# Kernel optimization log

Hardware: AMD Instinct MI355X
Metric: run time of the kernel (lower is better)

## Reference

```python
import jax, jax.numpy as jnp
import numpy as np

B, S, D, H = 4, 2048, 1024, 16
HD = D // H  # 64


def setup_inputs() -> dict:
    key = jax.random.key(0)
    k1, k2, k3 = jax.random.split(key, 3)
    return {
        "hidden_states": jax.random.normal(k1, (B, S, D), dtype=jnp.float32),
        "c_attn_w": jax.random.normal(k2, (D, 3 * D), dtype=jnp.float32) * 0.02,
        "c_attn_b": jnp.zeros((3 * D,), dtype=jnp.float32),
        "c_proj_w": jax.random.normal(k3, (D, D), dtype=jnp.float32) * 0.02,
        "c_proj_b": jnp.zeros((D,), dtype=jnp.float32),
    }


def reference(hidden_states, c_attn_w, c_attn_b, c_proj_w, c_proj_b):
    b, s, d = hidden_states.shape
    qkv = hidden_states @ c_attn_w + c_attn_b  # [B,S,3D]
    q, k, v = jnp.split(qkv, 3, axis=-1)
    # split heads -> [B,H,S,hd]
    def heads(x):
        return x.reshape(b, s, H, HD).transpose(0, 2, 1, 3)
    q, k, v = heads(q), heads(k), heads(v)
    scale = 1.0 / jnp.float32(HD) ** 0.5  # scale_attn_weights=True, no layer-idx scaling
    # fp32 scores (module forces float via autocast(False))
    w = jnp.einsum("bhqd,bhkd->bhqk", q.astype(jnp.float32), k.astype(jnp.float32)) * scale
    causal = jnp.tril(jnp.ones((s, s), dtype=bool))  # [S,S]
    mask_value = jnp.finfo(w.dtype).min
    w = jnp.where(causal[None, None], w, mask_value)
    w = jax.nn.softmax(w, axis=-1).astype(v.dtype)
    a = jnp.einsum("bhqk,bhkd->bhqd", w, v)  # [B,H,S,hd]
    a = a.transpose(0, 2, 1, 3).reshape(b, s, d)  # merge heads
    return a @ c_proj_w + c_proj_b
```

## Files before the change

kernel.cpp:

```cpp
#include <hip/hip_runtime.h>
#include <stdint.h>

typedef __bf16 bf16x8 __attribute__((ext_vector_type(8)));
typedef short s16x8 __attribute__((ext_vector_type(8)));
typedef float f32x4 __attribute__((ext_vector_type(4)));

__device__ __forceinline__ short f2bf(float f) {
  union { float f; uint32_t u; } c; c.f = f;
  uint32_t r = (c.u + 0x7fffu + ((c.u >> 16) & 1u)) >> 16;
  return (short)(uint16_t)r;
}

__device__ __forceinline__ void async_copy16(short* lds, const short* g) {
  __builtin_amdgcn_global_load_lds((const __attribute__((address_space(1))) void*)g,
                                   (__attribute__((address_space(3))) void*)lds,
                                   16, 0, 0);
}

__global__ __launch_bounds__(256) void cast_bf16_kernel(const float* __restrict__ in,
                                                        short* __restrict__ out) {
  int i = blockIdx.x * 256 + threadIdx.x;
  float4 v = reinterpret_cast<const float4*>(in)[i];
  short4 o;
  o.x = f2bf(v.x); o.y = f2bf(v.y); o.z = f2bf(v.z); o.w = f2bf(v.w);
  reinterpret_cast<short4*>(out)[i] = o;
}

__global__ __launch_bounds__(256) void transpose_cast_kernel(const float* __restrict__ in,
                                                             short* __restrict__ out,
                                                             int R, int C) {
  __shared__ float tile[32][33];
  int c0 = blockIdx.x * 32, r0 = blockIdx.y * 32;
  int tc = threadIdx.x & 31, tr = threadIdx.x >> 5;
#pragma unroll
  for (int p = 0; p < 4; ++p)
    tile[tr + p * 8][tc] = in[(size_t)(r0 + tr + p * 8) * C + c0 + tc];
  __syncthreads();
#pragma unroll
  for (int p = 0; p < 4; ++p)
    out[(size_t)(c0 + tr + p * 8) * R + r0 + tc] = f2bf(tile[tc][tr + p * 8]);
}

template <bool OBF, bool QSCALE>
__global__ __launch_bounds__(256) void gemm128_kernel(const short* __restrict__ A,
                                                      const short* __restrict__ Bt,
                                                      const float* __restrict__ bias,
                                                      void* __restrict__ Cout,
                                                      int K, int ldc) {
  __shared__ short Asm[128 * 32];
  __shared__ short Bsm[128 * 32];
  const int tid = threadIdx.x;
  const int lane = tid & 63, wid = tid >> 6;
  const int m0 = blockIdx.y * 128, n0 = blockIdx.x * 128;
  const int wm = wid >> 1, wn = wid & 1;
  const int lr = lane & 15, lg = lane >> 4;

  f32x4 acc[4][4] = {};

  const int s1 = tid, s2 = 256 + tid;
  const short* a1 = A + (size_t)(m0 + (s1 >> 2)) * K + (s1 & 3) * 8;
  const short* a2 = A + (size_t)(m0 + (s2 >> 2)) * K + (s2 & 3) * 8;
  const short* b1 = Bt + (size_t)(n0 + (s1 >> 2)) * K + (s1 & 3) * 8;
  const short* b2 = Bt + (size_t)(n0 + (s2 >> 2)) * K + (s2 & 3) * 8;

  for (int k0 = 0; k0 < K; k0 += 32) {
    __syncthreads();
    async_copy16(&Asm[s1 * 8], a1 + k0);
    async_copy16(&Asm[s2 * 8], a2 + k0);
    async_copy16(&Bsm[s1 * 8], b1 + k0);
    async_copy16(&Bsm[s2 * 8], b2 + k0);
    __syncthreads();

    bf16x8 af[4], bf[4];
#pragma unroll
    for (int mi = 0; mi < 4; ++mi)
      af[mi] = *(const bf16x8*)&Asm[(wm * 64 + mi * 16 + lr) * 32 + lg * 8];
#pragma unroll
    for (int ni = 0; ni < 4; ++ni)
      bf[ni] = *(const bf16x8*)&Bsm[(wn * 64 + ni * 16 + lr) * 32 + lg * 8];
    __builtin_amdgcn_s_setprio(1);
#pragma unroll
    for (int mi = 0; mi < 4; ++mi)
#pragma unroll
      for (int ni = 0; ni < 4; ++ni)
        acc[mi][ni] = __builtin_amdgcn_mfma_f32_16x16x32_bf16(af[mi], bf[ni], acc[mi][ni], 0, 0, 0);
    __builtin_amdgcn_s_setprio(0);
  }

#pragma unroll
  for (int ni = 0; ni < 4; ++ni) {
    const int col = n0 + wn * 64 + ni * 16 + lr;
    const float bv = bias[col];
    const float scale = (QSCALE && col < 1024) ? 0.18033688f : 1.0f;
#pragma unroll
    for (int mi = 0; mi < 4; ++mi) {
      const int row = m0 + wm * 64 + mi * 16 + lg * 4;
#pragma unroll
      for (int j = 0; j < 4; ++j) {
        const float v = (acc[mi][ni][j] + bv) * scale;
        if constexpr (OBF)
          ((short*)Cout)[(size_t)(row + j) * ldc + col] = f2bf(v);
        else
          ((float*)Cout)[(size_t)(row + j) * ldc + col] = v;
      }
    }
  }
}

__global__ __launch_bounds__(256) void vtrans_kernel(const short* __restrict__ qkv,
                                                     short* __restrict__ vt) {
  __shared__ short tile[64][72];
  const int tid = threadIdx.x;
  const int s0 = blockIdx.x * 64;
  const int h = blockIdx.y, b = blockIdx.z;
  const short* src = qkv + (size_t)(b * 2048 + s0) * 3072 + 2048 + h * 64;
#pragma unroll
  for (int p = 0; p < 2; ++p) {
    const int r = (tid >> 3) + p * 32;
    const int c0 = (tid & 7) * 8;
    *(s16x8*)&tile[r][c0] = *(const s16x8*)(src + (size_t)r * 3072 + c0);
  }
  __syncthreads();
  short* dst = vt + (size_t)(b * 16 + h) * 64 * 2048;
#pragma unroll
  for (int p = 0; p < 2; ++p) {
    const int d = (tid >> 3) + p * 32;
    const int sl0 = (tid & 7) * 8;
    s16x8 v;
#pragma unroll
    for (int i = 0; i < 8; ++i) v[i] = tile[sl0 + i][d];
    *(s16x8*)(dst + (size_t)d * 2048 + s0 + sl0) = v;
  }
}

__global__ __launch_bounds__(256) void attn_kernel(const short* __restrict__ qkv,
                                                   const short* __restrict__ vt,
                                                   short* __restrict__ abuf) {
  __shared__ short P_lds[4][32][72];
  const int tid = threadIdx.x;
  const int lane = tid & 63, wid = tid >> 6;
  const int lr = lane & 15, lg = lane >> 4;
  const int h = blockIdx.y, b = blockIdx.z;
  const int ldq = 3072;
  const short* Qb = qkv + (size_t)b * 2048 * ldq + h * 64;
  const short* Kb = Qb + 1024;
  const short* Vtb = vt + (size_t)(b * 16 + h) * 64 * 2048;

  for (int pp = 0; pp < 2; ++pp) {
    const int qtile = pp ? (int)blockIdx.x : 15 - (int)blockIdx.x;
    const int qrowA = qtile * 128 + wid * 32;

    bf16x8 qf[2][2];
#pragma unroll
    for (int qb = 0; qb < 2; ++qb)
#pragma unroll
      for (int g = 0; g < 2; ++g)
        qf[qb][g] = *(const bf16x8*)(Qb + (size_t)(qrowA + qb * 16 + lr) * ldq + g * 32 + lg * 8);

    f32x4 o[2][4] = {};
    float mst[2][4], lst[2][4];
#pragma unroll
    for (int qb = 0; qb < 2; ++qb)
#pragma unroll
      for (int j = 0; j < 4; ++j) { mst[qb][j] = -__builtin_inff(); lst[qb][j] = 0.f; }

    const int ntiles = ((qrowA + 31) >> 6) + 1;

    bf16x8 kf[4][2];
#pragma unroll
    for (int ni = 0; ni < 4; ++ni)
#pragma unroll
      for (int g = 0; g < 2; ++g)
        kf[ni][g] = *(const bf16x8*)(Kb + (size_t)(ni * 16 + lr) * ldq + g * 32 + lg * 8);

    for (int t = 0; t < ntiles; ++t) {
      const int kvt = t << 6;

      f32x4 s[2][4];
      __builtin_amdgcn_s_setprio(1);
#pragma unroll
      for (int qb = 0; qb < 2; ++qb)
#pragma unroll
        for (int ni = 0; ni < 4; ++ni) {
          f32x4 z = {0.f, 0.f, 0.f, 0.f};
          s[qb][ni] = z;
#pragma unroll
          for (int g = 0; g < 2; ++g)
            s[qb][ni] = __builtin_amdgcn_mfma_f32_16x16x32_bf16(qf[qb][g], kf[ni][g], s[qb][ni], 0, 0, 0);
        }
      __builtin_amdgcn_s_setprio(0);

      bf16x8 kn[4][2];
      if (t + 1 < ntiles) {
        const int kvn = kvt + 64;
#pragma unroll
        for (int ni = 0; ni < 4; ++ni)
#pragma unroll
          for (int g = 0; g < 2; ++g)
            kn[ni][g] = *(const bf16x8*)(Kb + (size_t)(kvn + ni * 16 + lr) * ldq + g * 32 + lg * 8);
      }
      bf16x8 vb[4][2];
#pragma unroll
      for (int db = 0; db < 4; ++db)
#pragma unroll
        for (int g = 0; g < 2; ++g)
          vb[db][g] = *(const bf16x8*)(Vtb + (size_t)(db * 16 + lr) * 2048 + kvt + g * 32 + lg * 8);

      if (kvt + 63 > qrowA) {
#pragma unroll
        for (int qb = 0; qb < 2; ++qb)
#pragma unroll
          for (int ni = 0; ni < 4; ++ni)
#pragma unroll
            for (int j = 0; j < 4; ++j) {
              const int q = qrowA + qb * 16 + lg * 4 + j;
              const int kv = kvt + ni * 16 + lr;
              if (kv > q) s[qb][ni][j] = -__builtin_inff();
            }
      }

      float alpha[2][4];
#pragma unroll
      for (int qb = 0; qb < 2; ++qb)
#pragma unroll
        for (int j = 0; j < 4; ++j) {
          float v = fmaxf(fmaxf(s[qb][0][j], s[qb][1][j]), fmaxf(s[qb][2][j], s[qb][3][j]));
          v = fmaxf(v, __shfl_xor(v, 1, 64));
          v = fmaxf(v, __shfl_xor(v, 2, 64));
          v = fmaxf(v, __shfl_xor(v, 4, 64));
          v = fmaxf(v, __shfl_xor(v, 8, 64));
          const float mn = fmaxf(mst[qb][j], v);
          alpha[qb][j] = exp2f(mst[qb][j] - mn);
          mst[qb][j] = mn;
          lst[qb][j] *= alpha[qb][j];
        }

#pragma unroll
      for (int qb = 0; qb < 2; ++qb)
#pragma unroll
        for (int db = 0; db < 4; ++db)
#pragma unroll
          for (int j = 0; j < 4; ++j)
            o[qb][db][j] *= alpha[qb][j];

      float psum[2][4] = {};
#pragma unroll
      for (int qb = 0; qb < 2; ++qb)
#pragma unroll
        for (int ni = 0; ni < 4; ++ni)
#pragma unroll
          for (int j = 0; j < 4; ++j) {
            const float p = exp2f(s[qb][ni][j] - mst[qb][j]);
            psum[qb][j] += p;
            P_lds[wid][qb * 16 + lg * 4 + j][ni * 16 + lr] = f2bf(p);
          }
#pragma unroll
      for (int qb = 0; qb < 2; ++qb)
#pragma unroll
        for (int j = 0; j < 4; ++j) {
          float v = psum[qb][j];
          v += __shfl_xor(v, 1, 64);
          v += __shfl_xor(v, 2, 64);
          v += __shfl_xor(v, 4, 64);
          v += __shfl_xor(v, 8, 64);
          lst[qb][j] += v;
        }

      bf16x8 pa[2][2];
#pragma unroll
      for (int qb = 0; qb < 2; ++qb)
#pragma unroll
        for (int g = 0; g < 2; ++g)
          pa[qb][g] = *(const bf16x8*)&P_lds[wid][qb * 16 + lr][g * 32 + lg * 8];

      __builtin_amdgcn_s_setprio(1);
#pragma unroll
      for (int qb = 0; qb < 2; ++qb)
#pragma unroll
        for (int db = 0; db < 4; ++db)
#pragma unroll
          for (int g = 0; g < 2; ++g)
            o[qb][db] = __builtin_amdgcn_mfma_f32_16x16x32_bf16(pa[qb][g], vb[db][g], o[qb][db], 0, 0, 0);
      __builtin_amdgcn_s_setprio(0);

#pragma unroll
      for (int ni = 0; ni < 4; ++ni)
#pragma unroll
        for (int g = 0; g < 2; ++g)
          kf[ni][g] = kn[ni][g];
    }

#pragma unroll
    for (int qb = 0; qb < 2; ++qb) {
      float rl[4];
#pragma unroll
      for (int j = 0; j < 4; ++j) rl[j] = 1.0f / lst[qb][j];
#pragma unroll
      for (int db = 0; db < 4; ++db) {
        const int col = h * 64 + db * 16 + lr;
#pragma unroll
        for (int j = 0; j < 4; ++j) {
          const int row = b * 2048 + qrowA + qb * 16 + lg * 4 + j;
          abuf[(size_t)row * 1024 + col] = f2bf(o[qb][db][j] * rl[j]);
        }
      }
    }
  }
}

extern "C" void kernel_launch(void* const* d_in, const int* in_sizes, int n_in,
                              void* d_out, int out_size, void* d_ws, size_t ws_size,
                              hipStream_t stream) {
  (void)in_sizes; (void)n_in; (void)out_size; (void)ws_size;
  const float* hs = (const float*)d_in[0];
  const float* w1 = (const float*)d_in[1];
  const float* b1 = (const float*)d_in[2];
  const float* w2 = (const float*)d_in[3];
  const float* b2 = (const float*)d_in[4];

  char* w = (char*)d_ws;
  short* Xb  = (short*)(w);
  short* W1T = (short*)(w + 16777216);
  short* W2T = (short*)(w + 23068672);
  short* QKV = (short*)(w + 25165824);
  short* VT  = (short*)(w + 75497472);
  short* AB  = (short*)(w + 92274688);

  cast_bf16_kernel<<<8192, 256, 0, stream>>>(hs, Xb);
  transpose_cast_kernel<<<dim3(96, 32), 256, 0, stream>>>(w1, W1T, 1024, 3072);
  transpose_cast_kernel<<<dim3(32, 32), 256, 0, stream>>>(w2, W2T, 1024, 1024);
  gemm128_kernel<true, true><<<dim3(24, 64), 256, 0, stream>>>(Xb, W1T, b1, QKV, 1024, 3072);
  vtrans_kernel<<<dim3(32, 16, 4), 256, 0, stream>>>(QKV, VT);
  attn_kernel<<<dim3(8, 16, 4), 256, 0, stream>>>(QKV, VT, AB);
  gemm128_kernel<false, false><<<dim3(8, 64), 256, 0, stream>>>(AB, W2T, b2, d_out, 1024, 1024);
}
```

Baseline: 388.9 us.

## Halve attention query tile per wave, remap grid, add lazy softmax rescaling

The attention kernel now gives each wave 16 query rows instead of 32, with each block covering a pair of 64-row subtiles. This doubles the grid to 1024 blocks, and a swizzled 1D block index maps blocks to (batch, head, tile) so that neighbouring blocks spread across heads. The online softmax now skips rescaling the max and the accumulators unless some row's max grows by more than 8 (log2 units), which removes exp and multiply work on most tiles. The bf16 conversion uses the native cast instead of manual rounding. The trade-offs are that K and V are reloaded per 16 rows, which doubles the global traffic for K and V, and that the lazy rescale depends on the bounded growth of the scores.

```diff
diff --git a/kernel.cpp b/kernel.cpp
--- a/kernel.cpp
+++ b/kernel.cpp
@@ -6,9 +6,9 @@
 typedef float f32x4 __attribute__((ext_vector_type(4)));
 
 __device__ __forceinline__ short f2bf(float f) {
-  union { float f; uint32_t u; } c; c.f = f;
-  uint32_t r = (c.u + 0x7fffu + ((c.u >> 16) & 1u)) >> 16;
-  return (short)(uint16_t)r;
+  union { __bf16 h; short s; } u;
+  u.h = (__bf16)f;
+  return u.s;
 }
 
 __device__ __forceinline__ void async_copy16(short* lds, const short* g) {
@@ -136,58 +136,56 @@
 __global__ __launch_bounds__(256) void attn_kernel(const short* __restrict__ qkv,
                                                    const short* __restrict__ vt,
                                                    short* __restrict__ abuf) {
-  __shared__ short P_lds[4][32][72];
+  __shared__ short P_lds[4][16][72];
   const int tid = threadIdx.x;
   const int lane = tid & 63, wid = tid >> 6;
   const int lr = lane & 15, lg = lane >> 4;
-  const int h = blockIdx.y, b = blockIdx.z;
+
+  const int g = blockIdx.x;
+  const int w = ((g & 7) << 7) | (g >> 3);
+  const int px = w & 15, h = (w >> 4) & 15, b = w >> 8;
+
   const int ldq = 3072;
   const short* Qb = qkv + (size_t)b * 2048 * ldq + h * 64;
   const short* Kb = Qb + 1024;
   const short* Vtb = vt + (size_t)(b * 16 + h) * 64 * 2048;
 
   for (int pp = 0; pp < 2; ++pp) {
-    const int qtile = pp ? (int)blockIdx.x : 15 - (int)blockIdx.x;
-    const int qrowA = qtile * 128 + wid * 32;
-
-    bf16x8 qf[2][2];
-#pragma unroll
-    for (int qb = 0; qb < 2; ++qb)
-#pragma unroll
-      for (int g = 0; g < 2; ++g)
-        qf[qb][g] = *(const bf16x8*)(Qb + (size_t)(qrowA + qb * 16 + lr) * ldq + g * 32 + lg * 8);
-
-    f32x4 o[2][4] = {};
-    float mst[2][4], lst[2][4];
-#pragma unroll
-    for (int qb = 0; qb < 2; ++qb)
-#pragma unroll
-      for (int j = 0; j < 4; ++j) { mst[qb][j] = -__builtin_inff(); lst[qb][j] = 0.f; }
-
-    const int ntiles = ((qrowA + 31) >> 6) + 1;
+    const int qsub = pp ? px : 31 - px;
+    const int qrowA = qsub * 64 + wid * 16;
+
+    bf16x8 qf[2];
+#pragma unroll
+    for (int gg = 0; gg < 2; ++gg)
+      qf[gg] = *(const bf16x8*)(Qb + (size_t)(qrowA + lr) * ldq + gg * 32 + lg * 8);
+
+    f32x4 o[4] = {};
+    float mst[4], lst[4];
+#pragma unroll
+    for (int j = 0; j < 4; ++j) { mst[j] = -__builtin_inff(); lst[j] = 0.f; }
+
+    const int ntiles = qsub + 1;
 
     bf16x8 kf[4][2];
 #pragma unroll
     for (int ni = 0; ni < 4; ++ni)
 #pragma unroll
-      for (int g = 0; g < 2; ++g)
-        kf[ni][g] = *(const bf16x8*)(Kb + (size_t)(ni * 16 + lr) * ldq + g * 32 + lg * 8);
+      for (int gg = 0; gg < 2; ++gg)
+        kf[ni][gg] = *(const bf16x8*)(Kb + (size_t)(ni * 16 + lr) * ldq + gg * 32 + lg * 8);
 
     for (int t = 0; t < ntiles; ++t) {
       const int kvt = t << 6;
 
-      f32x4 s[2][4];
+      f32x4 s[4];
       __builtin_amdgcn_s_setprio(1);
 #pragma unroll
-      for (int qb = 0; qb < 2; ++qb)
-#pragma unroll
-        for (int ni = 0; ni < 4; ++ni) {
-          f32x4 z = {0.f, 0.f, 0.f, 0.f};
-          s[qb][ni] = z;
-#pragma unroll
-          for (int g = 0; g < 2; ++g)
-            s[qb][ni] = __builtin_amdgcn_mfma_f32_16x16x32_bf16(qf[qb][g], kf[ni][g], s[qb][ni], 0, 0, 0);
-        }
+      for (int ni = 0; ni < 4; ++ni) {
+        f32x4 z = {0.f, 0.f, 0.f, 0.f};
+        s[ni] = z;
+#pragma unroll
+        for (int gg = 0; gg < 2; ++gg)
+          s[ni] = __builtin_amdgcn_mfma_f32_16x16x32_bf16(qf[gg], kf[ni][gg], s[ni], 0, 0, 0);
+      }
       __builtin_amdgcn_s_setprio(0);
 
       bf16x8 kn[4][2];
@@ -196,113 +194,101 @@
 #pragma unroll
         for (int ni = 0; ni < 4; ++ni)
 #pragma unroll
-          for (int g = 0; g < 2; ++g)
-            kn[ni][g] = *(const bf16x8*)(Kb + (size_t)(kvn + ni * 16 + lr) * ldq + g * 32 + lg * 8);
+          for (int gg = 0; gg < 2; ++gg)
+            kn[ni][gg] = *(const bf16x8*)(Kb + (size_t)(kvn + ni * 16 + lr) * ldq + gg * 32 + lg * 8);
       }
       bf16x8 vb[4][2];
 #pragma unroll
       for (int db = 0; db < 4; ++db)
 #pragma unroll
-        for (int g = 0; g < 2; ++g)
-          vb[db][g] = *(const bf16x8*)(Vtb + (size_t)(db * 16 + lr) * 2048 + kvt + g * 32 + lg * 8);
+        for (int gg = 0; gg < 2; ++gg)
+          vb[db][gg] = *(const bf16x8*)(Vtb + (size_t)(db * 16 + lr) * 2048 + kvt + gg * 32 + lg * 8);
 
       if (kvt + 63 > qrowA) {
 #pragma unroll
-        for (int qb = 0; qb < 2; ++qb)
-#pragma unroll
-          for (int ni = 0; ni < 4; ++ni)
-#pragma unroll
-            for (int j = 0; j < 4; ++j) {
-              const int q = qrowA + qb * 16 + lg * 4 + j;
-              const int kv = kvt + ni * 16 + lr;
-              if (kv > q) s[qb][ni][j] = -__builtin_inff();
-            }
-      }
-
-      float alpha[2][4];
-#pragma unroll
-      for (int qb = 0; qb < 2; ++qb)
+        for (int ni = 0; ni < 4; ++ni)
+#pragma unroll
+          for (int j = 0; j < 4; ++j) {
+            const int q = qrowA + lg * 4 + j;
+            const int kv = kvt + ni * 16 + lr;
+            if (kv > q) s[ni][j] = -__builtin_inff();
+          }
+      }
+
+      float v4[4];
+#pragma unroll
+      for (int j = 0; j < 4; ++j) {
+        float v = fmaxf(fmaxf(s[0][j], s[1][j]), fmaxf(s[2][j], s[3][j]));
+        v = fmaxf(v, __shfl_xor(v, 1, 64));
+        v = fmaxf(v, __shfl_xor(v, 2, 64));
+        v = fmaxf(v, __shfl_xor(v, 4, 64));
+        v = fmaxf(v, __shfl_xor(v, 8, 64));
+        v4[j] = v;
+      }
+      float gmax = fmaxf(fmaxf(v4[0] - mst[0], v4[1] - mst[1]),
+                         fmaxf(v4[2] - mst[2], v4[3] - mst[3]));
+      if (!__all(gmax <= 8.f)) {
 #pragma unroll
         for (int j = 0; j < 4; ++j) {
-          float v = fmaxf(fmaxf(s[qb][0][j], s[qb][1][j]), fmaxf(s[qb][2][j], s[qb][3][j]));
-          v = fmaxf(v, __shfl_xor(v, 1, 64));
-          v = fmaxf(v, __shfl_xor(v, 2, 64));
-          v = fmaxf(v, __shfl_xor(v, 4, 64));
-          v = fmaxf(v, __shfl_xor(v, 8, 64));
-          const float mn = fmaxf(mst[qb][j], v);
-          alpha[qb][j] = exp2f(mst[qb][j] - mn);
-          mst[qb][j] = mn;
-          lst[qb][j] *= alpha[qb][j];
+          const float mn = fmaxf(mst[j], v4[j]);
+          const float alpha = exp2f(mst[j] - mn);
+          mst[j] = mn;
+          lst[j] *= alpha;
+#pragma unroll
+          for (int db = 0; db < 4; ++db)
+            o[db][j] *= alpha;
         }
-
-#pragma unroll
-      for (int qb = 0; qb < 2; ++qb)
-#pragma unroll
-        for (int db = 0; db < 4; ++db)
-#pragma unroll
-          for (int j = 0; j < 4; ++j)
-            o[qb][db][j] *= alpha[qb][j];
-
-      float psum[2][4] = {};
-#pragma unroll
-      for (int qb = 0; qb < 2; ++qb)
-#pragma unroll
-        for (int ni = 0; ni < 4; ++ni)
-#pragma unroll
-          for (int j = 0; j < 4; ++j) {
-            const float p = exp2f(s[qb][ni][j] - mst[qb][j]);
-            psum[qb][j] += p;
-            P_lds[wid][qb * 16 + lg * 4 + j][ni * 16 + lr] = f2bf(p);
-          }
-#pragma unroll
-      for (int qb = 0; qb < 2; ++qb)
+      }
+
+      float psum[4] = {};
+#pragma unroll
+      for (int ni = 0; ni < 4; ++ni)
 #pragma unroll
         for (int j = 0; j < 4; ++j) {
-          float v = psum[qb][j];
-          v += __shfl_xor(v, 1, 64);
-          v += __shfl_xor(v, 2, 64);
-          v += __shfl_xor(v, 4, 64);
-          v += __shfl_xor(v, 8, 64);
-          lst[qb][j] += v;
+          const float p = exp2f(s[ni][j] - mst[j]);
+          psum[j] += p;
+          P_lds[wid][lg * 4 + j][ni * 16 + lr] = f2bf(p);
         }
-
-      bf16x8 pa[2][2];
-#pragma unroll
-      for (int qb = 0; qb < 2; ++qb)
-#pragma unroll
-        for (int g = 0; g < 2; ++g)
-          pa[qb][g] = *(const bf16x8*)&P_lds[wid][qb * 16 + lr][g * 32 + lg * 8];
+#pragma unroll
+      for (int j = 0; j < 4; ++j) {
+        float v = psum[j];
+        v += __shfl_xor(v, 1, 64);
+        v += __shfl_xor(v, 2, 64);
+        v += __shfl_xor(v, 4, 64);
+        v += __shfl_xor(v, 8, 64);
+        lst[j] += v;
+      }
+
+      bf16x8 pa[2];
+#pragma unroll
+      for (int gg = 0; gg < 2; ++gg)
+        pa[gg] = *(const bf16x8*)&P_lds[wid][lr][gg * 32 + lg * 8];
 
       __builtin_amdgcn_s_setprio(1);
 #pragma unroll
-      for (int qb = 0; qb < 2; ++qb)
-#pragma unroll
-        for (int db = 0; db < 4; ++db)
-#pragma unroll
-          for (int g = 0; g < 2; ++g)
-            o[qb][db] = __builtin_amdgcn_mfma_f32_16x16x32_bf16(pa[qb][g], vb[db][g], o[qb][db], 0, 0, 0);
+      for (int db = 0; db < 4; ++db)
+#pragma unroll
+        for (int gg = 0; gg < 2; ++gg)
+          o[db] = __builtin_amdgcn_mfma_f32_16x16x32_bf16(pa[gg], vb[db][gg], o[db], 0, 0, 0);
       __builtin_amdgcn_s_setprio(0);
 
 #pragma unroll
       for (int ni = 0; ni < 4; ++ni)
 #pragma unroll
-        for (int g = 0; g < 2; ++g)
-          kf[ni][g] = kn[ni][g];
+        for (int gg = 0; gg < 2; ++gg)
+          kf[ni][gg] = kn[ni][gg];
     }
 
-#pragma unroll
-    for (int qb = 0; qb < 2; ++qb) {
-      float rl[4];
-#pragma unroll
-      for (int j = 0; j < 4; ++j) rl[j] = 1.0f / lst[qb][j];
-#pragma unroll
-      for (int db = 0; db < 4; ++db) {
-        const int col = h * 64 + db * 16 + lr;
-#pragma unroll
-        for (int j = 0; j < 4; ++j) {
-          const int row = b * 2048 + qrowA + qb * 16 + lg * 4 + j;
-          abuf[(size_t)row * 1024 + col] = f2bf(o[qb][db][j] * rl[j]);
-        }
+    float rl[4];
+#pragma unroll
+    for (int j = 0; j < 4; ++j) rl[j] = 1.0f / lst[j];
+#pragma unroll
+    for (int db = 0; db < 4; ++db) {
+      const int col = h * 64 + db * 16 + lr;
+#pragma unroll
+      for (int j = 0; j < 4; ++j) {
+        const int row = b * 2048 + qrowA + lg * 4 + j;
+        abuf[(size_t)row * 1024 + col] = f2bf(o[db][j] * rl[j]);
       }
     }
   }
@@ -331,6 +317,6 @@
   transpose_cast_kernel<<<dim3(32, 32), 256, 0, stream>>>(w2, W2T, 1024, 1024);
   gemm128_kernel<true, true><<<dim3(24, 64), 256, 0, stream>>>(Xb, W1T, b1, QKV, 1024, 3072);
   vtrans_kernel<<<dim3(32, 16, 4), 256, 0, stream>>>(QKV, VT);
-  attn_kernel<<<dim3(8, 16, 4), 256, 0, stream>>>(QKV, VT, AB);
+  attn_kernel<<<1024, 256, 0, stream>>>(QKV, VT, AB);
   gemm128_kernel<false, false><<<dim3(8, 64), 256, 0, stream>>>(AB, W2T, b2, d_out, 1024, 1024);
 }
```

After: 437.6 us. 1.13x slower.

## Add lazy softmax rescaling, XCD-aware block remap, and hardware bf16 conversion

Applied to the files above, without the earlier changes.

The attention kernel now skips the running-max update and output rescale unless some row's new max exceeds the stored max by more than 8 (in log2 units), checked wave-wide with __all. This removes per-tile exp2 and accumulator multiplies in the common case. In exchange, the unnormalised probabilities may grow up to 2^8 before rescaling, which could cost bf16 precision. The grid is also flattened to 1D with a swizzle that places related heads/batches on the same XCD for L2 locality, and f2bf now uses the compiler's native bf16 conversion instead of manual rounding.

```diff
diff --git a/kernel.cpp b/kernel.cpp
--- a/kernel.cpp
+++ b/kernel.cpp
@@ -6,9 +6,9 @@
 typedef float f32x4 __attribute__((ext_vector_type(4)));
 
 __device__ __forceinline__ short f2bf(float f) {
-  union { float f; uint32_t u; } c; c.f = f;
-  uint32_t r = (c.u + 0x7fffu + ((c.u >> 16) & 1u)) >> 16;
-  return (short)(uint16_t)r;
+  union { __bf16 h; short s; } u;
+  u.h = (__bf16)f;
+  return u.s;
 }
 
 __device__ __forceinline__ void async_copy16(short* lds, const short* g) {
@@ -140,22 +140,26 @@
   const int tid = threadIdx.x;
   const int lane = tid & 63, wid = tid >> 6;
   const int lr = lane & 15, lg = lane >> 4;
-  const int h = blockIdx.y, b = blockIdx.z;
+
+  const int g = blockIdx.x;
+  const int w = ((g & 7) << 6) | (g >> 3);
+  const int px = w & 7, h = (w >> 3) & 15, b = w >> 7;
+
   const int ldq = 3072;
   const short* Qb = qkv + (size_t)b * 2048 * ldq + h * 64;
   const short* Kb = Qb + 1024;
   const short* Vtb = vt + (size_t)(b * 16 + h) * 64 * 2048;
 
   for (int pp = 0; pp < 2; ++pp) {
-    const int qtile = pp ? (int)blockIdx.x : 15 - (int)blockIdx.x;
+    const int qtile = pp ? px : 15 - px;
     const int qrowA = qtile * 128 + wid * 32;
 
     bf16x8 qf[2][2];
 #pragma unroll
     for (int qb = 0; qb < 2; ++qb)
 #pragma unroll
-      for (int g = 0; g < 2; ++g)
-        qf[qb][g] = *(const bf16x8*)(Qb + (size_t)(qrowA + qb * 16 + lr) * ldq + g * 32 + lg * 8);
+      for (int gg = 0; gg < 2; ++gg)
+        qf[qb][gg] = *(const bf16x8*)(Qb + (size_t)(qrowA + qb * 16 + lr) * ldq + gg * 32 + lg * 8);
 
     f32x4 o[2][4] = {};
     float mst[2][4], lst[2][4];
@@ -170,8 +174,8 @@
 #pragma unroll
     for (int ni = 0; ni < 4; ++ni)
 #pragma unroll
-      for (int g = 0; g < 2; ++g)
-        kf[ni][g] = *(const bf16x8*)(Kb + (size_t)(ni * 16 + lr) * ldq + g * 32 + lg * 8);
+      for (int gg = 0; gg < 2; ++gg)
+        kf[ni][gg] = *(const bf16x8*)(Kb + (size_t)(ni * 16 + lr) * ldq + gg * 32 + lg * 8);
 
     for (int t = 0; t < ntiles; ++t) {
       const int kvt = t << 6;
@@ -185,8 +189,8 @@
           f32x4 z = {0.f, 0.f, 0.f, 0.f};
           s[qb][ni] = z;
 #pragma unroll
-          for (int g = 0; g < 2; ++g)
-            s[qb][ni] = __builtin_amdgcn_mfma_f32_16x16x32_bf16(qf[qb][g], kf[ni][g], s[qb][ni], 0, 0, 0);
+          for (int gg = 0; gg < 2; ++gg)
+            s[qb][ni] = __builtin_amdgcn_mfma_f32_16x16x32_bf16(qf[qb][gg], kf[ni][gg], s[qb][ni], 0, 0, 0);
         }
       __builtin_amdgcn_s_setprio(0);
 
@@ -196,15 +200,15 @@
 #pragma unroll
         for (int ni = 0; ni < 4; ++ni)
 #pragma unroll
-          for (int g = 0; g < 2; ++g)
-            kn[ni][g] = *(const bf16x8*)(Kb + (size_t)(kvn + ni * 16 + lr) * ldq + g * 32 + lg * 8);
+          for (int gg = 0; gg < 2; ++gg)
+            kn[ni][gg] = *(const bf16x8*)(Kb + (size_t)(kvn + ni * 16 + lr) * ldq + gg * 32 + lg * 8);
       }
       bf16x8 vb[4][2];
 #pragma unroll
       for (int db = 0; db < 4; ++db)
 #pragma unroll
-        for (int g = 0; g < 2; ++g)
-          vb[db][g] = *(const bf16x8*)(Vtb + (size_t)(db * 16 + lr) * 2048 + kvt + g * 32 + lg * 8);
+        for (int gg = 0; gg < 2; ++gg)
+          vb[db][gg] = *(const bf16x8*)(Vtb + (size_t)(db * 16 + lr) * 2048 + kvt + gg * 32 + lg * 8);
 
       if (kvt + 63 > qrowA) {
 #pragma unroll
@@ -219,7 +223,7 @@
             }
       }
 
-      float alpha[2][4];
+      float v4[2][4];
 #pragma unroll
       for (int qb = 0; qb < 2; ++qb)
 #pragma unroll
@@ -229,19 +233,27 @@
           v = fmaxf(v, __shfl_xor(v, 2, 64));
           v = fmaxf(v, __shfl_xor(v, 4, 64));
           v = fmaxf(v, __shfl_xor(v, 8, 64));
-          const float mn = fmaxf(mst[qb][j], v);
-          alpha[qb][j] = exp2f(mst[qb][j] - mn);
-          mst[qb][j] = mn;
-          lst[qb][j] *= alpha[qb][j];
+          v4[qb][j] = v;
         }
-
-#pragma unroll
-      for (int qb = 0; qb < 2; ++qb)
-#pragma unroll
-        for (int db = 0; db < 4; ++db)
-#pragma unroll
-          for (int j = 0; j < 4; ++j)
-            o[qb][db][j] *= alpha[qb][j];
+      float gmax = -__builtin_inff();
+#pragma unroll
+      for (int qb = 0; qb < 2; ++qb)
+#pragma unroll
+        for (int j = 0; j < 4; ++j) gmax = fmaxf(gmax, v4[qb][j] - mst[qb][j]);
+      if (!__all(gmax <= 8.f)) {
+#pragma unroll
+        for (int qb = 0; qb < 2; ++qb)
+#pragma unroll
+          for (int j = 0; j < 4; ++j) {
+            const float mn = fmaxf(mst[qb][j], v4[qb][j]);
+            const float alpha = exp2f(mst[qb][j] - mn);
+            mst[qb][j] = mn;
+            lst[qb][j] *= alpha;
+#pragma unroll
+            for (int db = 0; db < 4; ++db)
+              o[qb][db][j] *= alpha;
+          }
+      }
 
       float psum[2][4] = {};
 #pragma unroll
@@ -270,8 +282,8 @@
 #pragma unroll
       for (int qb = 0; qb < 2; ++qb)
 #pragma unroll
-        for (int g = 0; g < 2; ++g)
-          pa[qb][g] = *(const bf16x8*)&P_lds[wid][qb * 16 + lr][g * 32 + lg * 8];
+        for (int gg = 0; gg < 2; ++gg)
+          pa[qb][gg] = *(const bf16x8*)&P_lds[wid][qb * 16 + lr][gg * 32 + lg * 8];
 
       __builtin_amdgcn_s_setprio(1);
 #pragma unroll
@@ -279,15 +291,15 @@
 #pragma unroll
         for (int db = 0; db < 4; ++db)
 #pragma unroll
-          for (int g = 0; g < 2; ++g)
-            o[qb][db] = __builtin_amdgcn_mfma_f32_16x16x32_bf16(pa[qb][g], vb[db][g], o[qb][db], 0, 0, 0);
+          for (int gg = 0; gg < 2; ++gg)
+            o[qb][db] = __builtin_amdgcn_mfma_f32_16x16x32_bf16(pa[qb][gg], vb[db][gg], o[qb][db], 0, 0, 0);
       __builtin_amdgcn_s_setprio(0);
 
 #pragma unroll
       for (int ni = 0; ni < 4; ++ni)
 #pragma unroll
-        for (int g = 0; g < 2; ++g)
-          kf[ni][g] = kn[ni][g];
+        for (int gg = 0; gg < 2; ++gg)
+          kf[ni][gg] = kn[ni][gg];
     }
 
 #pragma unroll
@@ -331,6 +343,6 @@
   transpose_cast_kernel<<<dim3(32, 32), 256, 0, stream>>>(w2, W2T, 1024, 1024);
   gemm128_kernel<true, true><<<dim3(24, 64), 256, 0, stream>>>(Xb, W1T, b1, QKV, 1024, 3072);
   vtrans_kernel<<<dim3(32, 16, 4), 256, 0, stream>>>(QKV, VT);
-  attn_kernel<<<dim3(8, 16, 4), 256, 0, stream>>>(QKV, VT, AB);
+  attn_kernel<<<512, 256, 0, stream>>>(QKV, VT, AB);
   gemm128_kernel<false, false><<<dim3(8, 64), 256, 0, stream>>>(AB, W2T, b2, d_out, 1024, 1024);
 }
```

New measurement: 370.5 us. 4.7% less time.
